# Optimization experiments

Hardware: AMD Instinct MI355X
Metric: run time of the kernel (lower is better)

Reference implementation:

```python
import jax, jax.numpy as jnp
import numpy as np

LOG2 = 0.6931471805599453

def ssp(x):
    # ShiftedSoftplus: softplus(x) - ln(2)
    return jax.nn.softplus(x) - LOG2

N_ATOMS = 100000
N_PAIRS = 1600000
F_ATOM = 128   # number_of_per_atom_features
F_FILT = 128   # number_of_filters
N_RBF = 32     # number_of_radial_basis_functions

def setup_inputs() -> dict:
    key = jax.random.key(0)
    ks = jax.random.split(key, 12)
    s = lambda k, fan_in, shape: jax.random.normal(k, shape, dtype=jnp.float32) / np.sqrt(fan_in)
    return {
        "x": jax.random.normal(ks[0], (N_ATOMS, F_ATOM), dtype=jnp.float32),
        "pairlist": jax.random.randint(ks[1], (2, N_PAIRS), 0, N_ATOMS),
        "f_ij": jax.random.uniform(ks[2], (N_PAIRS, 1, N_RBF), dtype=jnp.float32),
        "f_ij_cutoff": jax.random.uniform(ks[3], (N_PAIRS, 1), dtype=jnp.float32),
        # intput_to_feature: Dense(F_ATOM -> F_FILT, bias=False)
        "W_in": s(ks[4], F_ATOM, (F_ATOM, F_FILT)),
        # filter_network: Dense(N_RBF -> F_FILT, SSP), Dense(F_FILT -> F_FILT)
        "Wf1": s(ks[5], N_RBF, (N_RBF, F_FILT)),
        "bf1": jnp.zeros((F_FILT,), dtype=jnp.float32),
        "Wf2": s(ks[6], F_FILT, (F_FILT, F_FILT)),
        "bf2": jnp.zeros((F_FILT,), dtype=jnp.float32),
        # feature_to_output: Dense(F_FILT -> F_ATOM, SSP), Dense(F_ATOM -> F_ATOM)
        "Wo1": s(ks[7], F_FILT, (F_FILT, F_ATOM)),
        "bo1": jnp.zeros((F_ATOM,), dtype=jnp.float32),
        "Wo2": s(ks[8], F_ATOM, (F_ATOM, F_ATOM)),
        "bo2": jnp.zeros((F_ATOM,), dtype=jnp.float32),
    }

def reference(x, pairlist, f_ij, f_ij_cutoff, W_in, Wf1, bf1, Wf2, bf2, Wo1, bo1, Wo2, bo2):
    idx_i, idx_j = pairlist[0], pairlist[1]
    # input projection (no bias)
    h = x @ W_in                                   # [N, F_FILT]
    # filter network on radial basis, modulated by cutoff
    W_ij = ssp(f_ij[:, 0, :] @ Wf1 + bf1) @ Wf2 + bf2   # [P, F_FILT]
    W_ij = W_ij * f_ij_cutoff                      # broadcast [P,1]
    # gather neighbor features, filter-weight, scatter-add per atom
    x_ij = h[idx_j] * W_ij                         # [P, F_FILT]
    out = jax.ops.segment_sum(x_ij, idx_i, num_segments=x.shape[0])
    # output MLP
    return ssp(out @ Wo1 + bo1) @ Wo2 + bo2        # [N, F_ATOM]
```

## Files before the change

### kernel.cpp

```cpp
#include <hip/hip_runtime.h>

#define NA   100000
#define NP   1600000
#define FDIM 128
#define NRBF 32
#define LN2  0.69314718055994530942f

typedef __attribute__((ext_vector_type(8))) short short8;
typedef __attribute__((ext_vector_type(4))) float f32x4;

__device__ __forceinline__ float ssp_f(float v) {
    float e = __builtin_amdgcn_exp2f(fabsf(v) * -1.4426950408889634f);
    float l = __builtin_amdgcn_logf(1.0f + e);
    return fmaxf(v, 0.0f) + 0.6931471805599453f * (l - 1.0f);
}

__device__ __forceinline__ short f2bf(float f) {
    union { float f; unsigned u; } v; v.f = f;
    unsigned r = v.u + 0x7FFF + ((v.u >> 16) & 1);
    return (short)(r >> 16);
}

__device__ __forceinline__ float bf2f(unsigned short u) {
    union { unsigned u; float f; } v; v.u = ((unsigned)u) << 16;
    return v.f;
}

__global__ void k_prep(const float* __restrict__ Wf1, const float* __restrict__ Wf2,
                       const float* __restrict__ Wo1, const float* __restrict__ Wo2,
                       const float* __restrict__ Win,
                       short* __restrict__ Wf1T, short* __restrict__ Wf2T,
                       short* __restrict__ Wo1T, short* __restrict__ Wo2T,
                       short* __restrict__ WinT) {
    int i = blockIdx.x * 256 + threadIdx.x;
    int n = i >> 7, k = i & 127;
    Wf2T[i] = f2bf(Wf2[k * FDIM + n]);
    Wo1T[i] = f2bf(Wo1[k * FDIM + n]);
    Wo2T[i] = f2bf(Wo2[k * FDIM + n]);
    WinT[i] = f2bf(Win[k * FDIM + n]);
    if (i < 128 * 32) {
        int n1 = i >> 5, k1 = i & 31;
        Wf1T[i] = f2bf(Wf1[k1 * FDIM + n1]);
    }
}

__global__ __launch_bounds__(256) void k_in_proj_mfma(
        const float* __restrict__ x, const short* __restrict__ WinT,
        short* __restrict__ hB,
        const int* __restrict__ pl, int* __restrict__ count) {
    __shared__ __attribute__((aligned(16))) unsigned short XsB[64 * 136];

    const int t = threadIdx.x;
    const int r0g = blockIdx.x * 64;
    const int lane = t & 63, wv = t >> 6, q = lane >> 4, ln = lane & 15;

    {
        int p = blockIdx.x * 1024 + t;
        #pragma unroll
        for (int i = 0; i < 4; ++i) {
            if (p < NP) atomicAdd(&count[pl[p]], 1);
            p += 256;
        }
    }

    #pragma unroll
    for (int i = 0; i < 4; ++i) {
        int idx = i * 256 + t;
        int row = idx >> 4, ch = idx & 15;
        float4 a = {0,0,0,0}, b = {0,0,0,0};
        if (r0g + row < NA) {
            const float* xp = x + (size_t)(r0g + row) * FDIM + ch * 8;
            a = *(const float4*)xp;
            b = *(const float4*)(xp + 4);
        }
        short8 s = {f2bf(a.x), f2bf(a.y), f2bf(a.z), f2bf(a.w),
                    f2bf(b.x), f2bf(b.y), f2bf(b.z), f2bf(b.w)};
        *(short8*)(XsB + row * 136 + ch * 8) = s;
    }
    __syncthreads();

    f32x4 c[8];
    #pragma unroll
    for (int tt = 0; tt < 8; ++tt) c[tt] = (f32x4){0.f, 0.f, 0.f, 0.f};
    #pragma unroll
    for (int kk = 0; kk < 4; ++kk) {
        short8 a = *(const short8*)(XsB + (16 * wv + ln) * 136 + kk * 32 + q * 8);
        #pragma unroll
        for (int tt = 0; tt < 8; ++tt) {
            short8 b = *(const short8*)(WinT + (16 * tt + ln) * FDIM + kk * 32 + q * 8);
            c[tt] = __builtin_amdgcn_mfma_f32_16x16x32_bf16(a, b, c[tt], 0, 0, 0);
        }
    }
    __syncthreads();

    #pragma unroll
    for (int tt = 0; tt < 8; ++tt)
        #pragma unroll
        for (int r = 0; r < 4; ++r)
            XsB[(16 * wv + 4 * q + r) * 136 + 16 * tt + ln] =
                (unsigned short)f2bf(c[tt][r]);
    __syncthreads();

    #pragma unroll
    for (int i = 0; i < 4; ++i) {
        int idx = i * 256 + t;
        int row = idx >> 4, ch = idx & 15;
        if (r0g + row < NA)
            *(short8*)(hB + (size_t)(r0g + row) * FDIM + ch * 8) =
                *(const short8*)(XsB + row * 136 + ch * 8);
    }
}

__global__ __launch_bounds__(256) void k_scan1(const int* __restrict__ count,
                                               int* __restrict__ base,
                                               int* __restrict__ bsum) {
    __shared__ int sh[256];
    int i = blockIdx.x * 256 + threadIdx.x;
    int v = (i < NA) ? count[i] : 0;
    sh[threadIdx.x] = v;
    __syncthreads();
    for (int off = 1; off < 256; off <<= 1) {
        int add = (threadIdx.x >= off) ? sh[threadIdx.x - off] : 0;
        __syncthreads();
        sh[threadIdx.x] += add;
        __syncthreads();
    }
    if (i < NA) base[i] = sh[threadIdx.x] - v;
    if (threadIdx.x == 255) bsum[blockIdx.x] = sh[255];
}

__global__ __launch_bounds__(512) void k_scan2(int* __restrict__ bsum, int nb) {
    __shared__ int sh[512];
    int t = threadIdx.x;
    int v = (t < nb) ? bsum[t] : 0;
    sh[t] = v;
    __syncthreads();
    for (int off = 1; off < 512; off <<= 1) {
        int add = (t >= off) ? sh[t - off] : 0;
        __syncthreads();
        sh[t] += add;
        __syncthreads();
    }
    if (t < nb) bsum[t] = sh[t] - v;
}

__global__ void k_scan3(const int* __restrict__ bsum, int* __restrict__ base,
                        int* __restrict__ cursor) {
    int i = blockIdx.x * 256 + threadIdx.x;
    if (i < NA) {
        int b = base[i] + bsum[blockIdx.x];
        base[i]   = b;
        cursor[i] = b;
    }
}

__global__ void k_reorder(const int* __restrict__ pl, int* __restrict__ cursor,
                          int* __restrict__ perm) {
    int p = blockIdx.x * 256 + threadIdx.x;
    if (p < NP) {
        int pos = atomicAdd(&cursor[pl[p]], 1);
        perm[pos] = p;
    }
}

__global__ __launch_bounds__(256) void k_pairs_mfma(
        const int*   __restrict__ perm,
        const int*   __restrict__ pl,
        const float* __restrict__ fij,
        const float* __restrict__ fcut,
        const short* __restrict__ hB,
        const short* __restrict__ Wf1T,
        const float* __restrict__ bf1,
        const short* __restrict__ Wf2T,
        const float* __restrict__ bf2,
        float* __restrict__ acc_out) {
    __shared__ float SlotAcc[64 * 132];
    unsigned short* TmpB = (unsigned short*)SlotAcc;
    __shared__ __attribute__((aligned(16))) unsigned short WB[64 * 136];
    __shared__ int   ajs[64], slots[64], slot_atom[64], sps_s[64];
    __shared__ float cuts[64];
    __shared__ int   nslots_s;

    const int t    = threadIdx.x;
    const int p0   = blockIdx.x * 64;
    const int lane = t & 63;
    const int wv   = t >> 6;
    const int q    = lane >> 4;
    const int ln   = lane & 15;

    if (t < 64) {
        int sp = perm[p0 + t];
        int ai = pl[sp];
        sps_s[t] = sp;
        ajs[t]   = pl[NP + sp];
        cuts[t]  = fcut[sp];
        int prev = __shfl_up(ai, 1);
        bool head = (t == 0) || (ai != prev);
        unsigned long long mask = __ballot(head);
        int slot = __popcll(mask & ((2ULL << t) - 1)) - 1;
        slots[t] = slot;
        if (head) slot_atom[slot] = ai;
        if (t == 0) nslots_s = (int)__popcll(mask);
    }
    __syncthreads();

    short8 aF;
    {
        const float* fr = fij + (size_t)sps_s[16 * wv + ln] * NRBF + q * 8;
        float4 f0 = *(const float4*)(fr);
        float4 f1 = *(const float4*)(fr + 4);
        aF = (short8){f2bf(f0.x), f2bf(f0.y), f2bf(f0.z), f2bf(f0.w),
                      f2bf(f1.x), f2bf(f1.y), f2bf(f1.z), f2bf(f1.w)};
    }
    f32x4 c1[8];
    #pragma unroll
    for (int tt = 0; tt < 8; ++tt) {
        short8 b = *(const short8*)(Wf1T + (16 * tt + ln) * NRBF + q * 8);
        f32x4 z = {0.f, 0.f, 0.f, 0.f};
        c1[tt] = __builtin_amdgcn_mfma_f32_16x16x32_bf16(aF, b, z, 0, 0, 0);
    }

    #pragma unroll
    for (int tt = 0; tt < 8; ++tt) {
        float bias = bf1[16 * tt + ln];
        #pragma unroll
        for (int r = 0; r < 4; ++r) {
            float v = ssp_f(c1[tt][r] + bias);
            TmpB[(16 * wv + 4 * q + r) * 136 + 16 * tt + ln] = (unsigned short)f2bf(v);
        }
    }
    __syncthreads();

    f32x4 c2[8];
    #pragma unroll
    for (int tt = 0; tt < 8; ++tt) c2[tt] = (f32x4){0.f, 0.f, 0.f, 0.f};
    #pragma unroll
    for (int kk = 0; kk < 4; ++kk) {
        short8 a = *(const short8*)(TmpB + (16 * wv + ln) * 136 + kk * 32 + q * 8);
        #pragma unroll
        for (int tt = 0; tt < 8; ++tt) {
            short8 b = *(const short8*)(Wf2T + (size_t)(16 * tt + ln) * FDIM + kk * 32 + q * 8);
            c2[tt] = __builtin_amdgcn_mfma_f32_16x16x32_bf16(a, b, c2[tt], 0, 0, 0);
        }
    }

    #pragma unroll
    for (int tt = 0; tt < 8; ++tt) {
        float bias = bf2[16 * tt + ln];
        #pragma unroll
        for (int r = 0; r < 4; ++r) {
            int row = 16 * wv + 4 * q + r;
            float v = (c2[tt][r] + bias) * cuts[row];
            WB[row * 136 + 16 * tt + ln] = (unsigned short)f2bf(v);
        }
    }
    __syncthreads();

    for (int i = t; i < 64 * 132; i += 256) SlotAcc[i] = 0.f;
    __syncthreads();

    {
        const int r0 = (t >> 4) * 4;
        const int c0 = (t & 15) * 8;
        float run[8] = {};
        int cur = slots[r0];
        #pragma unroll
        for (int r = 0; r < 4; ++r) {
            int p = r0 + r;
            int s = slots[p];
            if (s != cur) {
                #pragma unroll
                for (int j = 0; j < 8; ++j) {
                    atomicAdd(&SlotAcc[cur * 132 + c0 + j], run[j]);
                    run[j] = 0.f;
                }
                cur = s;
            }
            short8 wb = *(const short8*)(WB + p * 136 + c0);
            short8 hb = *(const short8*)(hB + (size_t)ajs[p] * FDIM + c0);
            #pragma unroll
            for (int j = 0; j < 8; ++j)
                run[j] = fmaf(bf2f((unsigned short)wb[j]),
                              bf2f((unsigned short)hb[j]), run[j]);
        }
        #pragma unroll
        for (int j = 0; j < 8; ++j)
            atomicAdd(&SlotAcc[cur * 132 + c0 + j], run[j]);
    }
    __syncthreads();

    const int nslots = nslots_s;
    const int c0 = (t & 15) * 8;
    for (int s = (t >> 4); s < nslots; s += 16) {
        float* outp = acc_out + (size_t)slot_atom[s] * FDIM + c0;
        const float* src = &SlotAcc[s * 132 + c0];
        if (s == 0 || s == nslots - 1) {
            #pragma unroll
            for (int j = 0; j < 8; ++j)
                unsafeAtomicAdd(outp + j, src[j]);
        } else {
            *(float4*)(outp)     = *(const float4*)(src);
            *(float4*)(outp + 4) = *(const float4*)(src + 4);
        }
    }
}

__global__ __launch_bounds__(256) void k_out_mfma(
        const float* __restrict__ acc_in,
        const short* __restrict__ Wo1T, const float* __restrict__ bo1,
        const short* __restrict__ Wo2T, const float* __restrict__ bo2,
        float* __restrict__ out) {
    __shared__ __attribute__((aligned(16))) char lds[64 * 136 * 2 * 2];
    unsigned short* AsB = (unsigned short*)lds;
    unsigned short* O1B = (unsigned short*)(lds + 64 * 136 * 2);
    float* Of = (float*)lds;

    const int t = threadIdx.x;
    const int r0g = blockIdx.x * 64;
    const int lane = t & 63, wv = t >> 6, q = lane >> 4, ln = lane & 15;

    #pragma unroll
    for (int i = 0; i < 4; ++i) {
        int idx = i * 256 + t;
        int row = idx >> 4, ch = idx & 15;
        float4 a = {0,0,0,0}, b = {0,0,0,0};
        if (r0g + row < NA) {
            const float* ap = acc_in + (size_t)(r0g + row) * FDIM + ch * 8;
            a = *(const float4*)ap;
            b = *(const float4*)(ap + 4);
        }
        short8 s = {f2bf(a.x), f2bf(a.y), f2bf(a.z), f2bf(a.w),
                    f2bf(b.x), f2bf(b.y), f2bf(b.z), f2bf(b.w)};
        *(short8*)(AsB + row * 136 + ch * 8) = s;
    }
    __syncthreads();

    f32x4 c1[8];
    #pragma unroll
    for (int tt = 0; tt < 8; ++tt) c1[tt] = (f32x4){0.f, 0.f, 0.f, 0.f};
    #pragma unroll
    for (int kk = 0; kk < 4; ++kk) {
        short8 a = *(const short8*)(AsB + (16 * wv + ln) * 136 + kk * 32 + q * 8);
        #pragma unroll
        for (int tt = 0; tt < 8; ++tt) {
            short8 b = *(const short8*)(Wo1T + (16 * tt + ln) * FDIM + kk * 32 + q * 8);
            c1[tt] = __builtin_amdgcn_mfma_f32_16x16x32_bf16(a, b, c1[tt], 0, 0, 0);
        }
    }
    #pragma unroll
    for (int tt = 0; tt < 8; ++tt) {
        float bias = bo1[16 * tt + ln];
        #pragma unroll
        for (int r = 0; r < 4; ++r) {
            float v = ssp_f(c1[tt][r] + bias);
            O1B[(16 * wv + 4 * q + r) * 136 + 16 * tt + ln] = (unsigned short)f2bf(v);
        }
    }
    __syncthreads();

    f32x4 c2[8];
    #pragma unroll
    for (int tt = 0; tt < 8; ++tt) c2[tt] = (f32x4){0.f, 0.f, 0.f, 0.f};
    #pragma unroll
    for (int kk = 0; kk < 4; ++kk) {
        short8 a = *(const short8*)(O1B + (16 * wv + ln) * 136 + kk * 32 + q * 8);
        #pragma unroll
        for (int tt = 0; tt < 8; ++tt) {
            short8 b = *(const short8*)(Wo2T + (16 * tt + ln) * FDIM + kk * 32 + q * 8);
            c2[tt] = __builtin_amdgcn_mfma_f32_16x16x32_bf16(a, b, c2[tt], 0, 0, 0);
        }
    }
    __syncthreads();

    #pragma unroll
    for (int tt = 0; tt < 8; ++tt) {
        float bias = bo2[16 * tt + ln];
        #pragma unroll
        for (int r = 0; r < 4; ++r)
            Of[(16 * wv + 4 * q + r) * 132 + 16 * tt + ln] = c2[tt][r] + bias;
    }
    __syncthreads();

    #pragma unroll
    for (int i = 0; i < 8; ++i) {
        int idx = i * 256 + t;
        int row = idx >> 5, ch = idx & 31;
        if (r0g + row < NA)
            *(float4*)(out + (size_t)(r0g + row) * FDIM + ch * 4) =
                *(const float4*)(Of + row * 132 + ch * 4);
    }
}

__global__ __launch_bounds__(256) void k_in_proj(const float* __restrict__ x,
                                                 const float* __restrict__ W,
                                                 float* __restrict__ h) {
    __shared__ float Xs[32 * 132];
    const int t  = threadIdx.x;
    const int r0g = blockIdx.x * 32;
    const float4* xv = (const float4*)(x + (size_t)r0g * FDIM);
    #pragma unroll
    for (int i = 0; i < 4; ++i) {
        int idx = t + i * 256;
        *(float4*)(&Xs[(idx >> 5) * 132 + (idx & 31) * 4]) = xv[idx];
    }
    __syncthreads();
    const int c0 = (t & 15) * 8;
    const int r0 = (t >> 4) * 2;
    float acc[2][8] = {};
    #pragma unroll 4
    for (int k = 0; k < FDIM; ++k) {
        float xa = Xs[r0 * 132 + k];
        float xb = Xs[(r0 + 1) * 132 + k];
        float4 w0 = *(const float4*)(W + k * FDIM + c0);
        float4 w1 = *(const float4*)(W + k * FDIM + c0 + 4);
        float wv[8] = {w0.x, w0.y, w0.z, w0.w, w1.x, w1.y, w1.z, w1.w};
        #pragma unroll
        for (int j = 0; j < 8; ++j) {
            acc[0][j] += xa * wv[j];
            acc[1][j] += xb * wv[j];
        }
    }
    #pragma unroll
    for (int i = 0; i < 2; ++i) {
        float4 o0 = {acc[i][0], acc[i][1], acc[i][2], acc[i][3]};
        float4 o1 = {acc[i][4], acc[i][5], acc[i][6], acc[i][7]};
        float* hp = h + (size_t)(r0g + r0 + i) * FDIM + c0;
        *(float4*)(hp) = o0;  *(float4*)(hp + 4) = o1;
    }
}

__global__ __launch_bounds__(256) void k_pairs(const int*   __restrict__ pl,
                                               const float* __restrict__ fij,
                                               const float* __restrict__ fcut,
                                               const float* __restrict__ h,
                                               const float* __restrict__ Wf1,
                                               const float* __restrict__ bf1,
                                               const float* __restrict__ Wf2,
                                               const float* __restrict__ bf2,
                                               float* __restrict__ acc_out) {
    __shared__ float Fs[64 * 36];
    __shared__ float Tmp[64 * 132];
    __shared__ int   pis[64], pjs[64];
    __shared__ float cuts[64];
    const int t  = threadIdx.x;
    const int p0 = blockIdx.x * 64;
    const float4* fv = (const float4*)(fij + (size_t)p0 * NRBF);
    #pragma unroll
    for (int i = 0; i < 2; ++i) {
        int idx = t + i * 256;
        *(float4*)(&Fs[(idx >> 3) * 36 + (idx & 7) * 4]) = fv[idx];
    }
    if (t < 64) {
        pis[t]  = pl[p0 + t];
        pjs[t]  = pl[NP + p0 + t];
        cuts[t] = fcut[p0 + t];
    }
    __syncthreads();
    const int c0 = (t & 15) * 8;
    const int r0 = (t >> 4) * 4;
    float a1[4][8] = {};
    #pragma unroll 4
    for (int k = 0; k < NRBF; ++k) {
        float4 w0 = *(const float4*)(Wf1 + k * FDIM + c0);
        float4 w1 = *(const float4*)(Wf1 + k * FDIM + c0 + 4);
        float wv[8] = {w0.x, w0.y, w0.z, w0.w, w1.x, w1.y, w1.z, w1.w};
        float xr[4];
        #pragma unroll
        for (int i = 0; i < 4; ++i) xr[i] = Fs[(r0 + i) * 36 + k];
        #pragma unroll
        for (int i = 0; i < 4; ++i)
            #pragma unroll
            for (int j = 0; j < 8; ++j)
                a1[i][j] += xr[i] * wv[j];
    }
    {
        float4 b0 = *(const float4*)(bf1 + c0);
        float4 b1 = *(const float4*)(bf1 + c0 + 4);
        float bv[8] = {b0.x, b0.y, b0.z, b0.w, b1.x, b1.y, b1.z, b1.w};
        #pragma unroll
        for (int i = 0; i < 4; ++i)
            #pragma unroll
            for (int j = 0; j < 8; ++j)
                Tmp[(r0 + i) * 132 + c0 + j] = ssp_f(a1[i][j] + bv[j]);
    }
    __syncthreads();
    float a2[4][8] = {};
    #pragma unroll 2
    for (int k = 0; k < FDIM; ++k) {
        float4 w0 = *(const float4*)(Wf2 + k * FDIM + c0);
        float4 w1 = *(const float4*)(Wf2 + k * FDIM + c0 + 4);
        float wv[8] = {w0.x, w0.y, w0.z, w0.w, w1.x, w1.y, w1.z, w1.w};
        float xr[4];
        #pragma unroll
        for (int i = 0; i < 4; ++i) xr[i] = Tmp[(r0 + i) * 132 + k];
        #pragma unroll
        for (int i = 0; i < 4; ++i)
            #pragma unroll
            for (int j = 0; j < 8; ++j)
                a2[i][j] += xr[i] * wv[j];
    }
    float4 b20 = *(const float4*)(bf2 + c0);
    float4 b21 = *(const float4*)(bf2 + c0 + 4);
    float bv[8] = {b20.x, b20.y, b20.z, b20.w, b21.x, b21.y, b21.z, b21.w};
    #pragma unroll
    for (int i = 0; i < 4; ++i) {
        int   p   = r0 + i;
        float cut = cuts[p];
        const float* hr = h + (size_t)pjs[p] * FDIM + c0;
        float4 h0 = *(const float4*)(hr);
        float4 h1 = *(const float4*)(hr + 4);
        float hv[8] = {h0.x, h0.y, h0.z, h0.w, h1.x, h1.y, h1.z, h1.w};
        float* outp = acc_out + (size_t)pis[p] * FDIM + c0;
        #pragma unroll
        for (int j = 0; j < 8; ++j)
            unsafeAtomicAdd(outp + j, (a2[i][j] + bv[j]) * cut * hv[j]);
    }
}

__global__ __launch_bounds__(256) void k_out(const float* __restrict__ acc_in,
                                             const float* __restrict__ Wo1,
                                             const float* __restrict__ bo1,
                                             const float* __restrict__ Wo2,
                                             const float* __restrict__ bo2,
                                             float* __restrict__ out) {
    __shared__ float As[32 * 132];
    __shared__ float O1[32 * 132];
    const int t   = threadIdx.x;
    const int r0g = blockIdx.x * 32;
    const float4* av = (const float4*)(acc_in + (size_t)r0g * FDIM);
    #pragma unroll
    for (int i = 0; i < 4; ++i) {
        int idx = t + i * 256;
        *(float4*)(&As[(idx >> 5) * 132 + (idx & 31) * 4]) = av[idx];
    }
    __syncthreads();
    const int c0 = (t & 15) * 8;
    const int r0 = (t >> 4) * 2;
    float acc[2][8] = {};
    #pragma unroll 4
    for (int k = 0; k < FDIM; ++k) {
        float xa = As[r0 * 132 + k];
        float xb = As[(r0 + 1) * 132 + k];
        float4 w0 = *(const float4*)(Wo1 + k * FDIM + c0);
        float4 w1 = *(const float4*)(Wo1 + k * FDIM + c0 + 4);
        float wv[8] = {w0.x, w0.y, w0.z, w0.w, w1.x, w1.y, w1.z, w1.w};
        #pragma unroll
        for (int j = 0; j < 8; ++j) {
            acc[0][j] += xa * wv[j];
            acc[1][j] += xb * wv[j];
        }
    }
    {
        float4 b0 = *(const float4*)(bo1 + c0);
        float4 b1 = *(const float4*)(bo1 + c0 + 4);
        float bv[8] = {b0.x, b0.y, b0.z, b0.w, b1.x, b1.y, b1.z, b1.w};
        #pragma unroll
        for (int i = 0; i < 2; ++i)
            #pragma unroll
            for (int j = 0; j < 8; ++j)
                O1[(r0 + i) * 132 + c0 + j] = ssp_f(acc[i][j] + bv[j]);
    }
    __syncthreads();
    float acc2[2][8] = {};
    #pragma unroll 4
    for (int k = 0; k < FDIM; ++k) {
        float xa = O1[r0 * 132 + k];
        float xb = O1[(r0 + 1) * 132 + k];
        float4 w0 = *(const float4*)(Wo2 + k * FDIM + c0);
        float4 w1 = *(const float4*)(Wo2 + k * FDIM + c0 + 4);
        float wv[8] = {w0.x, w0.y, w0.z, w0.w, w1.x, w1.y, w1.z, w1.w};
        #pragma unroll
        for (int j = 0; j < 8; ++j) {
            acc2[0][j] += xa * wv[j];
            acc2[1][j] += xb * wv[j];
        }
    }
    float4 b0 = *(const float4*)(bo2 + c0);
    float4 b1 = *(const float4*)(bo2 + c0 + 4);
    float bv[8] = {b0.x, b0.y, b0.z, b0.w, b1.x, b1.y, b1.z, b1.w};
    #pragma unroll
    for (int i = 0; i < 2; ++i) {
        float4 o0 = {acc2[i][0] + bv[0], acc2[i][1] + bv[1],
                     acc2[i][2] + bv[2], acc2[i][3] + bv[3]};
        float4 o1 = {acc2[i][4] + bv[4], acc2[i][5] + bv[5],
                     acc2[i][6] + bv[6], acc2[i][7] + bv[7]};
        float* op = out + (size_t)(r0g + r0 + i) * FDIM + c0;
        *(float4*)(op) = o0;  *(float4*)(op + 4) = o1;
    }
}

extern "C" void kernel_launch(void* const* d_in, const int* in_sizes, int n_in,
                              void* d_out, int out_size, void* d_ws, size_t ws_size,
                              hipStream_t stream) {
    const float* x    = (const float*)d_in[0];
    const int*   pl   = (const int*)  d_in[1];
    const float* fij  = (const float*)d_in[2];
    const float* fcut = (const float*)d_in[3];
    const float* W_in = (const float*)d_in[4];
    const float* Wf1  = (const float*)d_in[5];
    const float* bf1  = (const float*)d_in[6];
    const float* Wf2  = (const float*)d_in[7];
    const float* bf2  = (const float*)d_in[8];
    const float* Wo1  = (const float*)d_in[9];
    const float* bo1  = (const float*)d_in[10];
    const float* Wo2  = (const float*)d_in[11];
    const float* bo2  = (const float*)d_in[12];
    float* out = (float*)d_out;

    char*  wsp   = (char*)d_ws;
    float* acc   = (float*)wsp;
    short* hB    = (short*)(acc + (size_t)NA * FDIM);
    int*   count = (int*)(hB + (size_t)NA * FDIM);
    int*   base  = count + NA;
    int*   cursor= base + NA;
    int*   bsum  = cursor + NA;
    int*   perm  = bsum + 512;
    short* Wf1T  = (short*)(perm + NP);
    short* Wf2T  = Wf1T + 128 * 32;
    short* Wo1T  = Wf2T + 128 * 128;
    short* Wo2T  = Wo1T + 128 * 128;
    short* WinT  = Wo2T + 128 * 128;

    const size_t needed = (size_t)NA * FDIM * 4
                        + (size_t)NA * FDIM * 2
                        + ((size_t)NA * 3 + 512 + NP) * 4
                        + (size_t)(128 * 32 + 4 * 128 * 128) * 2;
    const bool sorted_path = (ws_size >= needed);

    const int NB  = (NA + 255) / 256;
    const int NBA = (NA + 63) / 64;

    if (sorted_path) {
        hipMemsetAsync(acc, 0, (size_t)NA * FDIM * sizeof(float), stream);
        hipMemsetAsync(count, 0, (size_t)NA * sizeof(int), stream);
        k_prep   <<<64, 256, 0, stream>>>(Wf1, Wf2, Wo1, Wo2, W_in,
                                          Wf1T, Wf2T, Wo1T, Wo2T, WinT);
        k_in_proj_mfma<<<NBA, 256, 0, stream>>>(x, WinT, hB, pl, count);
        k_scan1  <<<NB, 256, 0, stream>>>(count, base, bsum);
        k_scan2  <<<1, 512, 0, stream>>>(bsum, NB);
        k_scan3  <<<NB, 256, 0, stream>>>(bsum, base, cursor);
        k_reorder<<<(NP + 255) / 256, 256, 0, stream>>>(pl, cursor, perm);
        k_pairs_mfma<<<NP / 64, 256, 0, stream>>>(perm, pl, fij, fcut, hB,
                                                  Wf1T, bf1, Wf2T, bf2, acc);
        k_out_mfma<<<NBA, 256, 0, stream>>>(acc, Wo1T, bo1, Wo2T, bo2, out);
    } else {
        float* hF   = (float*)wsp;
        float* accF = hF + (size_t)NA * FDIM;
        hipMemsetAsync(accF, 0, (size_t)NA * FDIM * sizeof(float), stream);
        k_in_proj<<<NA / 32, 256, 0, stream>>>(x, W_in, hF);
        k_pairs<<<NP / 64, 256, 0, stream>>>(pl, fij, fcut, hF,
                                             Wf1, bf1, Wf2, bf2, accF);
        k_out<<<NA / 32, 256, 0, stream>>>(accF, Wo1, bo1, Wo2, bo2, out);
    }
}
```

Before: 1.387 ms.

## Prefetch neighbor features early and alias LDS buffers in pair kernel

The pair kernel now issues the gathered neighbor-feature loads (hB rows) and the pair indices straight from global memory into registers early, so they overlap the filter-network MFMA work instead of sitting after it. LDS usage shrinks by aliasing the WB filter buffer into the SlotAcc region and dropping the shared index arrays, and launch_bounds now requests 4 blocks per CU for higher occupancy. Only the slots actually used get zeroed. In exchange the kernel adds syncthreads barriers and holds more registers for the prefetched values, which could cost occupancy or create spills.

```diff
diff --git a/kernel.cpp b/kernel.cpp
--- a/kernel.cpp
+++ b/kernel.cpp
@@ -163,7 +163,7 @@
     }
 }
 
-__global__ __launch_bounds__(256) void k_pairs_mfma(
+__global__ __launch_bounds__(256, 4) void k_pairs_mfma(
         const int*   __restrict__ perm,
         const int*   __restrict__ pl,
         const float* __restrict__ fij,
@@ -174,10 +174,10 @@
         const short* __restrict__ Wf2T,
         const float* __restrict__ bf2,
         float* __restrict__ acc_out) {
-    __shared__ float SlotAcc[64 * 132];
+    __shared__ __attribute__((aligned(16))) float SlotAcc[64 * 136];
     unsigned short* TmpB = (unsigned short*)SlotAcc;
-    __shared__ __attribute__((aligned(16))) unsigned short WB[64 * 136];
-    __shared__ int   ajs[64], slots[64], slot_atom[64], sps_s[64];
+    unsigned short* WB   = (unsigned short*)SlotAcc + 64 * 136;
+    __shared__ int   slots[64], slot_atom[64];
     __shared__ float cuts[64];
     __shared__ int   nslots_s;
 
@@ -187,13 +187,18 @@
     const int wv   = t >> 6;
     const int q    = lane >> 4;
     const int ln   = lane & 15;
+    const int r0   = (t >> 4) * 4;
+    const int c0   = (t & 15) * 8;
+
+    const int sp_self = perm[p0 + 16 * wv + ln];
+    int pp[4];
+    #pragma unroll
+    for (int r = 0; r < 4; ++r) pp[r] = perm[p0 + r0 + r];
 
     if (t < 64) {
         int sp = perm[p0 + t];
         int ai = pl[sp];
-        sps_s[t] = sp;
-        ajs[t]   = pl[NP + sp];
-        cuts[t]  = fcut[sp];
+        cuts[t] = fcut[sp];
         int prev = __shfl_up(ai, 1);
         bool head = (t == 0) || (ai != prev);
         unsigned long long mask = __ballot(head);
@@ -202,11 +207,14 @@
         if (head) slot_atom[slot] = ai;
         if (t == 0) nslots_s = (int)__popcll(mask);
     }
-    __syncthreads();
+
+    int aj[4];
+    #pragma unroll
+    for (int r = 0; r < 4; ++r) aj[r] = pl[NP + pp[r]];
 
     short8 aF;
     {
-        const float* fr = fij + (size_t)sps_s[16 * wv + ln] * NRBF + q * 8;
+        const float* fr = fij + (size_t)sp_self * NRBF + q * 8;
         float4 f0 = *(const float4*)(fr);
         float4 f1 = *(const float4*)(fr + 4);
         aF = (short8){f2bf(f0.x), f2bf(f0.y), f2bf(f0.z), f2bf(f0.w),
@@ -229,7 +237,15 @@
             TmpB[(16 * wv + 4 * q + r) * 136 + 16 * tt + ln] = (unsigned short)f2bf(v);
         }
     }
-    __syncthreads();
+
+    short8 hreg[4];
+    #pragma unroll
+    for (int r = 0; r < 4; ++r)
+        hreg[r] = *(const short8*)(hB + (size_t)aj[r] * FDIM + c0);
+
+    __syncthreads();
+
+    const int nslots = nslots_s;
 
     f32x4 c2[8];
     #pragma unroll
@@ -243,6 +259,7 @@
             c2[tt] = __builtin_amdgcn_mfma_f32_16x16x32_bf16(a, b, c2[tt], 0, 0, 0);
         }
     }
+    __syncthreads();
 
     #pragma unroll
     for (int tt = 0; tt < 8; ++tt) {
@@ -256,44 +273,43 @@
     }
     __syncthreads();
 
-    for (int i = t; i < 64 * 132; i += 256) SlotAcc[i] = 0.f;
+    short8 wreg[4];
+    #pragma unroll
+    for (int r = 0; r < 4; ++r)
+        wreg[r] = *(const short8*)(WB + (r0 + r) * 136 + c0);
+    __syncthreads();
+
+    for (int i = t; i < nslots * 136; i += 256) SlotAcc[i] = 0.f;
     __syncthreads();
 
     {
-        const int r0 = (t >> 4) * 4;
-        const int c0 = (t & 15) * 8;
         float run[8] = {};
         int cur = slots[r0];
         #pragma unroll
         for (int r = 0; r < 4; ++r) {
-            int p = r0 + r;
-            int s = slots[p];
+            int s = slots[r0 + r];
             if (s != cur) {
                 #pragma unroll
                 for (int j = 0; j < 8; ++j) {
-                    atomicAdd(&SlotAcc[cur * 132 + c0 + j], run[j]);
+                    atomicAdd(&SlotAcc[cur * 136 + c0 + j], run[j]);
                     run[j] = 0.f;
                 }
                 cur = s;
             }
-            short8 wb = *(const short8*)(WB + p * 136 + c0);
-            short8 hb = *(const short8*)(hB + (size_t)ajs[p] * FDIM + c0);
             #pragma unroll
             for (int j = 0; j < 8; ++j)
-                run[j] = fmaf(bf2f((unsigned short)wb[j]),
-                              bf2f((unsigned short)hb[j]), run[j]);
+                run[j] = fmaf(bf2f((unsigned short)wreg[r][j]),
+                              bf2f((unsigned short)hreg[r][j]), run[j]);
         }
         #pragma unroll
         for (int j = 0; j < 8; ++j)
-            atomicAdd(&SlotAcc[cur * 132 + c0 + j], run[j]);
-    }
-    __syncthreads();
-
-    const int nslots = nslots_s;
-    const int c0 = (t & 15) * 8;
+            atomicAdd(&SlotAcc[cur * 136 + c0 + j], run[j]);
+    }
+    __syncthreads();
+
     for (int s = (t >> 4); s < nslots; s += 16) {
         float* outp = acc_out + (size_t)slot_atom[s] * FDIM + c0;
-        const float* src = &SlotAcc[s * 132 + c0];
+        const float* src = &SlotAcc[s * 136 + c0];
         if (s == 0 || s == nslots - 1) {
             #pragma unroll
             for (int j = 0; j < 8; ++j)
```

New measurement: 1.158 ms. -16.5%, faster.
